# Performance work log

Hardware: AMD Instinct MI355X
Metric: run time of the kernel (lower is better)

Reference implementation:

```python
import jax, jax.numpy as jnp
import numpy as np

N_ANCHORS = 9
OUTPUT_STRIDE = 16
TOP_N = 2000
NMS_IOU_THRESH = 0.7
MIN_SIZE = 0.01
EPS = 1e-7  # K.epsilon()


def setup_inputs() -> dict:
    key = jax.random.key(0)
    k1, k2 = jax.random.split(key)
    b, h, w = 8, 64, 64  # 1024px image / stride 16
    scores = jax.random.uniform(k1, (b, h, w, N_ANCHORS), jnp.float32)
    offsets = jax.random.normal(k2, (b, h, w, 4 * N_ANCHORS), jnp.float32) * 0.2
    scales = np.array([128.0, 256.0, 512.0])
    ratios = np.array([0.5, 1.0, 2.0])
    aw = (scales[:, None] * np.sqrt(ratios)[None, :]).reshape(-1)
    ah = (scales[:, None] / np.sqrt(ratios)[None, :]).reshape(-1)
    anchors = jnp.asarray(np.stack([aw, ah], axis=-1), jnp.float32)  # [9,2]
    return {"scores": scores, "offsets": offsets, "anchors": anchors}


def _pairwise_iou(a, b):
    # a: [N,4], b: [M,4] (x1,y1,x2,y2) -> [N,M]
    a = a[:, None, :]
    b = b[None, :, :]
    mins = jnp.maximum(a[..., :2], b[..., :2])
    maxs = jnp.minimum(a[..., 2:], b[..., 2:])
    wh = jnp.maximum(maxs - mins, 0.0)
    inter = wh[..., 0] * wh[..., 1]
    area_a = (a[..., 2] - a[..., 0]) * (a[..., 3] - a[..., 1])
    area_b = (b[..., 2] - b[..., 0]) * (b[..., 3] - b[..., 1])
    return inter / (area_a + area_b - inter + EPS)


def _nms_pad(boxes):
    # boxes: [N,4] already sorted by descending score (output of top_k).
    # Greedy NMS (matches tf.image.non_max_suppression semantics), keep order,
    # zero-pad suppressed tail (matches tf.pad to top_n in the original).
    N = boxes.shape[0]
    iou = _pairwise_iou(boxes, boxes)  # [N,N]
    idx = jnp.arange(N)

    def body(i, keep):
        suppress = keep[i] & (iou[i] > NMS_IOU_THRESH) & (idx > i)
        return keep & ~suppress

    keep = jax.lax.fori_loop(0, N, body, jnp.ones((N,), bool))
    sort_keys = jnp.where(keep, idx, N)          # kept indices first, in score order
    order = jnp.argsort(sort_keys)
    valid = (jnp.sort(sort_keys) < N).astype(boxes.dtype)
    return boxes[order] * valid[:, None]


def reference(scores, offsets, anchors):
    b, h, w, K = scores.shape
    off = offsets.reshape(b, h, w, K, 4)
    # anchor decode
    gx, gy = jnp.meshgrid(jnp.arange(w), jnp.arange(h))          # [h,w] each
    center = (jnp.stack([gx, gy], -1).astype(jnp.float32) + 0.5) * OUTPUT_STRIDE  # [h,w,2]
    center = center[:, :, None, :]                               # [h,w,1,2]
    img_wh = jnp.array([w, h], jnp.float32) * OUTPUT_STRIDE
    anc = anchors.reshape(1, 1, 1, K, 2)
    pred_wh = jnp.exp(off[..., 2:]) * anc / img_wh               # [b,h,w,K,2]
    pred_xcyc = (anc * off[..., :2] + center) / img_wh
    box5 = jnp.concatenate([pred_xcyc - pred_wh / 2.0,
                            pred_xcyc + pred_wh / 2.0,
                            scores[..., None]], axis=-1)         # [b,h,w,K,5]
    # filter: clip to [0,1], zero out tiny boxes
    box5 = jnp.clip(box5, 0.0, 1.0)
    wh = box5[..., 2:4] - box5[..., 0:2]
    valid = ((wh[..., 0] > MIN_SIZE) & (wh[..., 1] > MIN_SIZE)).astype(box5.dtype)
    box5 = box5 * valid[..., None]
    box5 = box5.reshape(b, -1, 5)                                # [b, h*w*K, 5]
    # per-image top-k by score, then NMS, then zero-pad to TOP_N
    _, top_i = jax.lax.top_k(box5[..., 4], TOP_N)                # [b, TOP_N]
    top_boxes = jnp.take_along_axis(box5[..., :4], top_i[..., None], axis=1)
    proposals = jax.vmap(_nms_pad)(top_boxes)                    # [b, TOP_N, 4]
    return proposals
```

## Files before the change

kernel.cpp:

```cpp
#include <hip/hip_runtime.h>
#include <stdint.h>

#pragma clang fp contract(off)

#define BATCH 8
#define HH 64
#define WW 64
#define KA 9
#define NBOX (HH * WW * KA)
#define TOPN 2000
#define NPAD 2048
#define NW 32
#define IOU_T 0.7f
#define MINSZ 0.01f
#define EPSF 1e-7f
#define TSTRIDE 33
#define CANDCAP 3072

typedef unsigned int u32;
typedef unsigned long long u64;

__device__ __forceinline__ float clamp01(float x) { return fminf(fmaxf(x, 0.0f), 1.0f); }

__device__ __forceinline__ void bar_lds()
{
    asm volatile("s_waitcnt lgkmcnt(0)" ::: "memory");
    __builtin_amdgcn_s_barrier();
}

__device__ __forceinline__ void decode_one(
    const float* __restrict__ scores, const float4* __restrict__ offsets,
    const float* __restrict__ anchors, int gid, int t,
    float4* boxOut, u32* keyOut)
{
    int k = t % KA;
    int pos = t / KA;
    int wx = pos & (WW - 1);
    int hy = pos >> 6;
    float s = scores[gid];
    float4 off = offsets[gid];
    float aw = anchors[2 * k], ah = anchors[2 * k + 1];
    float cx = ((float)wx + 0.5f) * 16.0f;
    float cy = ((float)hy + 0.5f) * 16.0f;
    float pw = (expf(off.z) * aw) / 1024.0f;
    float ph = (expf(off.w) * ah) / 1024.0f;
    float xc = (aw * off.x + cx) / 1024.0f;
    float yc = (ah * off.y + cy) / 1024.0f;
    float x1 = clamp01(xc - pw * 0.5f);
    float y1 = clamp01(yc - ph * 0.5f);
    float x2 = clamp01(xc + pw * 0.5f);
    float y2 = clamp01(yc + ph * 0.5f);
    float sc = clamp01(s);
    float m = ((x2 - x1) > MINSZ && (y2 - y1) > MINSZ) ? 1.0f : 0.0f;
    *boxOut = make_float4(x1 * m, y1 * m, x2 * m, y2 * m);
    *keyOut = __float_as_uint(sc * m);
}

__global__ __launch_bounds__(256) void zero_kernel(uint4* __restrict__ p, int n)
{
    int g = blockIdx.x * 256 + threadIdx.x;
    if (g < n) p[g] = make_uint4(0, 0, 0, 0);
}

__global__ __launch_bounds__(256) void decode_kernel(
    const float* __restrict__ scores, const float4* __restrict__ offsets,
    const float* __restrict__ anchors, u32* __restrict__ keys,
    u32* __restrict__ ghist)
{
    __shared__ u32 lhist[4096];
    for (int i = threadIdx.x; i < 4096; i += 256) lhist[i] = 0;
    __syncthreads();

    int gid = blockIdx.x * 256 + threadIdx.x;
    int b = gid / NBOX;
    int t = gid - b * NBOX;
    float4 box; u32 key;
    decode_one(scores, offsets, anchors, gid, t, &box, &key);
    keys[gid] = key;
    atomicAdd(&lhist[key >> 20], 1u);
    __syncthreads();

    for (int i = threadIdx.x; i < 4096; i += 256) {
        u32 v = lhist[i];
        if (v) atomicAdd(&ghist[(b << 12) + i], v);
    }
}

__device__ __forceinline__ void rank_find_4096(
    const u32* __restrict__ histL, u32* __restrict__ partial,
    int r, u32* Bsh, int* Rsh, int tid)
{
    partial[tid] = histL[4 * tid] + histL[4 * tid + 1]
                 + histL[4 * tid + 2] + histL[4 * tid + 3];
    __syncthreads();
    if (tid < 64) {
        int lane = tid;
        u32 s = 0;
#pragma unroll
        for (int q = 0; q < 16; ++q) s += partial[lane * 16 + q];
        u32 suf = s;
#pragma unroll
        for (int d = 1; d < 64; d <<= 1) {
            u32 t = __shfl_down(suf, d);
            if (lane + d < 64) suf += t;
        }
        u32 nxt = __shfl_down(suf, 1);
        if (lane == 63) nxt = 0;
        bool cross = (suf >= (u32)r) && (nxt < (u32)r);
        u64 bal = __ballot(cross);
        int L = (int)(__ffsll((unsigned long long)bal) - 1);
        u32 above = __shfl(nxt, L);
        u32 hv = histL[64 * L + lane];
        u32 suf2 = hv;
#pragma unroll
        for (int d = 1; d < 64; d <<= 1) {
            u32 t = __shfl_down(suf2, d);
            if (lane + d < 64) suf2 += t;
        }
        u32 nxt2 = __shfl_down(suf2, 1);
        if (lane == 63) nxt2 = 0;
        u32 mine2 = suf2 + above;
        nxt2 += above;
        if (mine2 >= (u32)r && nxt2 < (u32)r) {
            *Bsh = (u32)(64 * L + lane);
            *Rsh = r - (int)nxt2;
        }
    }
    __syncthreads();
}

__global__ __launch_bounds__(1024) void select_kernel(
    const u32* __restrict__ keys, const u32* __restrict__ ghist,
    const float* __restrict__ scores, const float4* __restrict__ offsets,
    const float* __restrict__ anchors, float4* __restrict__ topBoxes)
{
    int b = blockIdx.x;
    int tid = threadIdx.x;
    int lane = tid & 63;
    const u32* kb = keys + (size_t)b * NBOX;

    __shared__ u32 hist[4096];
    __shared__ u32 partial[1024];
    __shared__ u64 sel[NPAD];
    __shared__ u64 cand[CANDCAP];
    __shared__ u32 Bsh;
    __shared__ int Rsh;
    __shared__ int ctr, cctr;

    if (tid == 0) { ctr = 0; cctr = 0; }
    for (int i = tid; i < 4096; i += 1024) hist[i] = ghist[(b << 12) + i];
    for (int i = tid; i < NPAD; i += 1024) sel[i] = 0ull;
    __syncthreads();
    rank_find_4096(hist, partial, TOPN, &Bsh, &Rsh, tid);
    u32 P1 = Bsh;
    int r1 = Rsh;
    __syncthreads();

    const uint4* kb4 = (const uint4*)kb;
#pragma unroll 1
    for (int it = 0; it < NBOX / 4096; ++it) {
        int i4 = it * 1024 + tid;
        uint4 kv = kb4[i4];
        u32 karr[4] = { kv.x, kv.y, kv.z, kv.w };
        u64 bd[4], bc[4];
        int totd = 0, totc = 0;
#pragma unroll
        for (int q = 0; q < 4; ++q) {
            u32 top = karr[q] >> 20;
            bd[q] = __ballot(top > P1);
            bc[q] = __ballot(top == P1);
            totd += (int)__popcll(bd[q]);
            totc += (int)__popcll(bc[q]);
        }
        int based = 0, basec = 0;
        if (lane == 0) {
            if (totd) based = atomicAdd(&ctr, totd);
            if (totc) basec = atomicAdd(&cctr, totc);
        }
        based = __shfl(based, 0);
        basec = __shfl(basec, 0);
        u64 lmask = (1ull << lane) - 1ull;
        int offd = 0, offc = 0;
#pragma unroll
        for (int q = 0; q < 4; ++q) {
            u32 key = karr[q];
            int i = i4 * 4 + q;
            u64 K = ((u64)key << 16) | (u64)(0xFFFFu - (u32)i);
            u32 top = key >> 20;
            if (top > P1) {
                int slot = based + offd + (int)__popcll(bd[q] & lmask);
                if (slot < NPAD) sel[slot] = K;
            } else if (top == P1) {
                int cslot = basec + offc + (int)__popcll(bc[q] & lmask);
                if (cslot < CANDCAP) cand[cslot] = K;
            }
            offd += (int)__popcll(bd[q]);
            offc += (int)__popcll(bc[q]);
        }
    }
    __syncthreads();
    int cc = cctr < CANDCAP ? cctr : CANDCAP;

    u64 prefix = (u64)P1;
    int r = r1;
    for (int p = 0; p < 3; ++p) {
        int shift = 24 - 12 * p;
        for (int i = tid; i < 4096; i += 1024) hist[i] = 0;
        __syncthreads();
        for (int c = tid; c < cc; c += 1024) {
            u64 K = cand[c];
            if ((K >> (shift + 12)) == prefix)
                atomicAdd(&hist[(u32)((K >> shift) & 0xFFFull)], 1u);
        }
        __syncthreads();
        rank_find_4096(hist, partial, r, &Bsh, &Rsh, tid);
        prefix = (prefix << 12) | (u64)Bsh;
        r = Rsh;
        __syncthreads();
    }
    u64 T48 = prefix;

    for (int c = tid; c < cc; c += 1024) {
        u64 K = cand[c];
        bool take = (K >= T48);
        u64 bal = __ballot(take);
        int base = 0;
        if (lane == 0 && bal) base = atomicAdd(&ctr, (int)__popcll(bal));
        base = __shfl(base, 0);
        if (take) {
            int slot = base + (int)__popcll(bal & ((1ull << lane) - 1ull));
            if (slot < NPAD) sel[slot] = K;
        }
    }
    __syncthreads();

    u64 e0 = sel[tid];
    u64 e1 = sel[tid + 1024];
    const int i0 = tid, i1 = tid + 1024;

    for (int k = 2; k <= NPAD; k <<= 1) {
        for (int j = k >> 1; j >= 64; j >>= 1) {
            if (j == 1024) {
                u64 mx = e0 > e1 ? e0 : e1;
                u64 mn = e0 > e1 ? e1 : e0;
                e0 = mx; e1 = mn;
            } else {
                sel[i0] = e0; sel[i1] = e1;
                __syncthreads();
                u64 p0 = sel[i0 ^ j];
                u64 p1 = sel[i1 ^ j];
                bool kp0 = ((i0 & k) == 0) ^ ((i0 & j) != 0);
                bool kp1 = ((i1 & k) == 0) ^ ((i1 & j) != 0);
                e0 = kp0 ? (e0 > p0 ? e0 : p0) : (e0 < p0 ? e0 : p0);
                e1 = kp1 ? (e1 > p1 ? e1 : p1) : (e1 < p1 ? e1 : p1);
                __syncthreads();
            }
        }
        int jstart = (k >> 1) < 32 ? (k >> 1) : 32;
        for (int j = jstart; j >= 1; j >>= 1) {
            u64 p0 = __shfl_xor(e0, j);
            u64 p1 = __shfl_xor(e1, j);
            bool kp0 = ((i0 & k) == 0) ^ ((i0 & j) != 0);
            bool kp1 = ((i1 & k) == 0) ^ ((i1 & j) != 0);
            e0 = kp0 ? (e0 > p0 ? e0 : p0) : (e0 < p0 ? e0 : p0);
            e1 = kp1 ? (e1 > p1 ? e1 : p1) : (e1 < p1 ? e1 : p1);
        }
    }

    {
        float4 v; u32 kd;
        int idx = 0xFFFF - (int)(e0 & 0xFFFFull);
        decode_one(scores, offsets, anchors, b * NBOX + idx, idx, &v, &kd);
        topBoxes[b * NPAD + i0] = v;
    }
    {
        float4 v = make_float4(0, 0, 0, 0);
        if (i1 < TOPN) {
            u32 kd;
            int idx = 0xFFFF - (int)(e1 & 0xFFFFull);
            decode_one(scores, offsets, anchors, b * NBOX + idx, idx, &v, &kd);
        }
        topBoxes[b * NPAD + i1] = v;
    }
}

__global__ __launch_bounds__(256) void iou_kernel(
    const float4* __restrict__ topBoxes, u64* __restrict__ sup)
{
    int gid = blockIdx.x * 256 + threadIdx.x;
    int wid = gid >> 6;
    int lane = gid & 63;
    int b = wid / TOPN;
    int r = wid - b * TOPN;

    float4 A = topBoxes[(size_t)b * NPAD + r];
    float areaA = (A.z - A.x) * (A.w - A.y);
    size_t supBase = ((size_t)b * NPAD + r) * NW;

    for (int w = r >> 6; w < NW; ++w) {
        int j = w * 64 + lane;
        float4 Bx = topBoxes[(size_t)b * NPAD + j];
        float ix1 = fmaxf(A.x, Bx.x);
        float iy1 = fmaxf(A.y, Bx.y);
        float ix2 = fminf(A.z, Bx.z);
        float iy2 = fminf(A.w, Bx.w);
        float iw = fmaxf(ix2 - ix1, 0.0f);
        float ih = fmaxf(iy2 - iy1, 0.0f);
        float inter = iw * ih;
        float areaB = (Bx.z - Bx.x) * (Bx.w - Bx.y);
        float iou = inter / (areaA + areaB - inter + EPSF);
        bool s = (iou > IOU_T) && (j > r) && (j < TOPN);
        u64 m = __ballot(s);
        if (lane == 0) sup[supBase + w] = m;
    }
}

__global__ __launch_bounds__(256) void resolve_kernel(
    const u64* __restrict__ sup, const float4* __restrict__ topBoxes,
    float4* __restrict__ out)
{
    int b = blockIdx.x;
    int tid = threadIdx.x;
    __shared__ u64 tile[2][64 * TSTRIDE];
    __shared__ u64 keep[NW];
    __shared__ u64 nzmap[NW];
    __shared__ int wbase[NW];
    if (tid < NW) keep[tid] = (tid < 31) ? ~0ull : 0xFFFFull;
    const u64* supB = sup + (size_t)b * NPAD * NW;
    unsigned* keep32 = (unsigned*)keep;

    int row = tid >> 2;
    int wcol = (tid & 3) * 8;

    {
        const uint4* src = (const uint4*)(supB + tid * 8);
        uint4 p0 = src[0], p1 = src[1], p2 = src[2], p3 = src[3];
        u64* d = &tile[0][row * TSTRIDE + wcol];
        d[0] = ((u64)p0.y << 32) | p0.x;  d[1] = ((u64)p0.w << 32) | p0.z;
        d[2] = ((u64)p1.y << 32) | p1.x;  d[3] = ((u64)p1.w << 32) | p1.z;
        d[4] = ((u64)p2.y << 32) | p2.x;  d[5] = ((u64)p2.w << 32) | p2.z;
        d[6] = ((u64)p3.y << 32) | p3.x;  d[7] = ((u64)p3.w << 32) | p3.z;
    }
    bar_lds();

    for (int w = 0; w < NW; ++w) {
        int buf = w & 1;
        uint4 n0, n1, n2, n3;
        if (w + 1 < NW) {
            const uint4* src = (const uint4*)(supB + (size_t)(w + 1) * 2048 + tid * 8);
            n0 = src[0]; n1 = src[1]; n2 = src[2]; n3 = src[3];
        }

        if (tid < 64) {
            u64 m = tile[buf][tid * TSTRIDE + w];
            u64 later = 0;
            for (int w2 = w + 1; w2 < NW; ++w2) later |= tile[buf][tid * TSTRIDE + w2];
            u64 nzAny = __ballot((m | later) != 0ull);
            u64 nzDiag = __ballot(m != 0ull);
            u32 mlo = (u32)m, mhi = (u32)(m >> 32);
            u64 kw64 = keep[w];
            u32 kwlo = (u32)__builtin_amdgcn_readfirstlane((int)(u32)kw64);
            u32 kwhi = (u32)__builtin_amdgcn_readfirstlane((int)(u32)(kw64 >> 32));
            u64 kw = ((u64)kwhi << 32) | kwlo;
            u64 rem = kw & nzDiag;
            while (rem) {
                int t2 = (int)(__ffsll((unsigned long long)rem) - 1);
                u32 alo = (u32)__builtin_amdgcn_readlane((int)mlo, t2);
                u32 ahi = (u32)__builtin_amdgcn_readlane((int)mhi, t2);
                u64 mt = ((u64)ahi << 32) | alo;
                kw &= ~mt;
                rem &= ~(mt | (1ull << t2));
            }
            if (tid == 0) { keep[w] = kw; nzmap[w] = nzAny; }
        }
        bar_lds();

        u64 gate = keep[w] & nzmap[w];
        int w2 = tid & 31;
        int grp = tid >> 5;
        if (w2 > w && gate) {
            u64 acc = 0;
#pragma unroll
            for (int q = 0; q < 8; ++q) {
                int rl = grp * 8 + q;
                if ((gate >> rl) & 1ull)
                    acc |= tile[buf][rl * TSTRIDE + w2];
            }
            if (acc) {
                u32 lo = (u32)acc, hi = (u32)(acc >> 32);
                if (lo) atomicAnd(&keep32[2 * w2], ~lo);
                if (hi) atomicAnd(&keep32[2 * w2 + 1], ~hi);
            }
        }

        if (w + 1 < NW) {
            u64* d = &tile[buf ^ 1][row * TSTRIDE + wcol];
            d[0] = ((u64)n0.y << 32) | n0.x;  d[1] = ((u64)n0.w << 32) | n0.z;
            d[2] = ((u64)n1.y << 32) | n1.x;  d[3] = ((u64)n1.w << 32) | n1.z;
            d[4] = ((u64)n2.y << 32) | n2.x;  d[5] = ((u64)n2.w << 32) | n2.z;
            d[6] = ((u64)n3.y << 32) | n3.x;  d[7] = ((u64)n3.w << 32) | n3.z;
        }
        bar_lds();
    }

    if (tid == 0) {
        int s = 0;
        for (int w2 = 0; w2 < NW; ++w2) { wbase[w2] = s; s += __popcll(keep[w2]); }
    }
    __syncthreads();
    for (int i = tid; i < TOPN; i += 256)
        out[(size_t)b * TOPN + i] = make_float4(0, 0, 0, 0);
    __syncthreads();
    for (int i = tid; i < TOPN; i += 256) {
        int wi = i >> 6, bz = i & 63;
        u64 kw = keep[wi];
        if ((kw >> bz) & 1ull) {
            int pos = wbase[wi] + __popcll(kw & ((1ull << bz) - 1ull));
            out[(size_t)b * TOPN + pos] = topBoxes[(size_t)b * NPAD + i];
        }
    }
}

extern "C" void kernel_launch(void* const* d_in, const int* in_sizes, int n_in,
                              void* d_out, int out_size, void* d_ws, size_t ws_size,
                              hipStream_t stream)
{
    const float*  scores  = (const float*)d_in[0];
    const float4* offsets = (const float4*)d_in[1];
    const float*  anchors = (const float*)d_in[2];
    float4* out = (float4*)d_out;

    char* ws = (char*)d_ws;
    u64*    sup      = (u64*)(ws);
    u32*    keys     = (u32*)(ws + 4194304);
    float4* topBoxes = (float4*)(ws + 5373952);
    u32*    ghist    = (u32*)(ws + 5636096);

    zero_kernel<<<(131072 / 16 + 255) / 256, 256, 0, stream>>>((uint4*)ghist, 131072 / 16);
    decode_kernel<<<(BATCH * NBOX) / 256, 256, 0, stream>>>(scores, offsets, anchors, keys, ghist);
    select_kernel<<<BATCH, 1024, 0, stream>>>(keys, ghist, scores, offsets, anchors, topBoxes);
    iou_kernel<<<(BATCH * TOPN * 64) / 256, 256, 0, stream>>>(topBoxes, sup);
    resolve_kernel<<<BATCH, 256, 0, stream>>>(sup, topBoxes, out);
}
```

Measured before the change: 106.4 us.

## Split select kernel into scan, grid-wide compaction, and final refine kernels

The single per-image select kernel (8 blocks) is replaced by three kernels. A small scan kernel finds the top radix bucket, a compact kernel over 288 blocks filters keys into global selected and candidate buffers using global atomics, and a final kernel refines the threshold and sorts. The aim is to spread the memory-bound key scan across many CUs instead of 8. In exchange it adds two launches, global atomics, and a global round trip for the candidates, and the zeroed workspace region grows.

```diff
diff --git a/kernel.cpp b/kernel.cpp
--- a/kernel.cpp
+++ b/kernel.cpp
@@ -15,7 +15,7 @@
 #define MINSZ 0.01f
 #define EPSF 1e-7f
 #define TSTRIDE 33
-#define CANDCAP 3072
+#define CANDCAP 4096
 
 typedef unsigned int u32;
 typedef unsigned long long u64;
@@ -129,77 +129,98 @@
     __syncthreads();
 }
 
-__global__ __launch_bounds__(1024) void select_kernel(
-    const u32* __restrict__ keys, const u32* __restrict__ ghist,
+__global__ __launch_bounds__(1024) void scan_kernel(
+    const u32* __restrict__ ghist, u32* __restrict__ P, int* __restrict__ R)
+{
+    int b = blockIdx.x, tid = threadIdx.x;
+    __shared__ u32 hist[4096];
+    __shared__ u32 partial[1024];
+    __shared__ u32 Bsh;
+    __shared__ int Rsh;
+    for (int i = tid; i < 4096; i += 1024) hist[i] = ghist[(b << 12) + i];
+    __syncthreads();
+    rank_find_4096(hist, partial, TOPN, &Bsh, &Rsh, tid);
+    if (tid == 0) { P[b] = Bsh; R[b] = Rsh; }
+}
+
+__global__ __launch_bounds__(256) void compact_kernel(
+    const u32* __restrict__ keys, const u32* __restrict__ P,
+    int* __restrict__ ctr, int* __restrict__ cctr,
+    u64* __restrict__ selKeys, u64* __restrict__ candG)
+{
+    int bid = blockIdx.x;
+    int b = bid / 36;
+    int blk = bid - b * 36;
+    int tid = threadIdx.x;
+    int lane = tid & 63;
+    u32 P1 = P[b];
+
+    int i4 = blk * 256 + tid;
+    const uint4* kb4 = (const uint4*)(keys + (size_t)b * NBOX);
+    uint4 kv = kb4[i4];
+    u32 karr[4] = { kv.x, kv.y, kv.z, kv.w };
+    u64 bd[4], bc[4];
+    int totd = 0, totc = 0;
+#pragma unroll
+    for (int q = 0; q < 4; ++q) {
+        u32 top = karr[q] >> 20;
+        bd[q] = __ballot(top > P1);
+        bc[q] = __ballot(top == P1);
+        totd += (int)__popcll(bd[q]);
+        totc += (int)__popcll(bc[q]);
+    }
+    int based = 0, basec = 0;
+    if (lane == 0) {
+        if (totd) based = atomicAdd(&ctr[b], totd);
+        if (totc) basec = atomicAdd(&cctr[b], totc);
+    }
+    based = __shfl(based, 0);
+    basec = __shfl(basec, 0);
+    u64 lmask = (1ull << lane) - 1ull;
+    int offd = 0, offc = 0;
+#pragma unroll
+    for (int q = 0; q < 4; ++q) {
+        u32 key = karr[q];
+        int i = i4 * 4 + q;
+        u64 K = ((u64)key << 16) | (u64)(0xFFFFu - (u32)i);
+        u32 top = key >> 20;
+        if (top > P1) {
+            int slot = based + offd + (int)__popcll(bd[q] & lmask);
+            if (slot < NPAD) selKeys[(size_t)b * NPAD + slot] = K;
+        } else if (top == P1) {
+            int cslot = basec + offc + (int)__popcll(bc[q] & lmask);
+            if (cslot < CANDCAP) candG[(size_t)b * CANDCAP + cslot] = K;
+        }
+        offd += (int)__popcll(bd[q]);
+        offc += (int)__popcll(bc[q]);
+    }
+}
+
+__global__ __launch_bounds__(1024) void final_kernel(
+    const u64* __restrict__ selKeysG, const u64* __restrict__ candG,
+    const u32* __restrict__ P, const int* __restrict__ R,
+    const int* __restrict__ ctr, const int* __restrict__ cctr,
     const float* __restrict__ scores, const float4* __restrict__ offsets,
     const float* __restrict__ anchors, float4* __restrict__ topBoxes)
 {
     int b = blockIdx.x;
     int tid = threadIdx.x;
     int lane = tid & 63;
-    const u32* kb = keys + (size_t)b * NBOX;
 
     __shared__ u32 hist[4096];
     __shared__ u32 partial[1024];
     __shared__ u64 sel[NPAD];
-    __shared__ u64 cand[CANDCAP];
     __shared__ u32 Bsh;
     __shared__ int Rsh;
-    __shared__ int ctr, cctr;
-
-    if (tid == 0) { ctr = 0; cctr = 0; }
-    for (int i = tid; i < 4096; i += 1024) hist[i] = ghist[(b << 12) + i];
-    for (int i = tid; i < NPAD; i += 1024) sel[i] = 0ull;
-    __syncthreads();
-    rank_find_4096(hist, partial, TOPN, &Bsh, &Rsh, tid);
-    u32 P1 = Bsh;
-    int r1 = Rsh;
-    __syncthreads();
-
-    const uint4* kb4 = (const uint4*)kb;
-#pragma unroll 1
-    for (int it = 0; it < NBOX / 4096; ++it) {
-        int i4 = it * 1024 + tid;
-        uint4 kv = kb4[i4];
-        u32 karr[4] = { kv.x, kv.y, kv.z, kv.w };
-        u64 bd[4], bc[4];
-        int totd = 0, totc = 0;
-#pragma unroll
-        for (int q = 0; q < 4; ++q) {
-            u32 top = karr[q] >> 20;
-            bd[q] = __ballot(top > P1);
-            bc[q] = __ballot(top == P1);
-            totd += (int)__popcll(bd[q]);
-            totc += (int)__popcll(bc[q]);
-        }
-        int based = 0, basec = 0;
-        if (lane == 0) {
-            if (totd) based = atomicAdd(&ctr, totd);
-            if (totc) basec = atomicAdd(&cctr, totc);
-        }
-        based = __shfl(based, 0);
-        basec = __shfl(basec, 0);
-        u64 lmask = (1ull << lane) - 1ull;
-        int offd = 0, offc = 0;
-#pragma unroll
-        for (int q = 0; q < 4; ++q) {
-            u32 key = karr[q];
-            int i = i4 * 4 + q;
-            u64 K = ((u64)key << 16) | (u64)(0xFFFFu - (u32)i);
-            u32 top = key >> 20;
-            if (top > P1) {
-                int slot = based + offd + (int)__popcll(bd[q] & lmask);
-                if (slot < NPAD) sel[slot] = K;
-            } else if (top == P1) {
-                int cslot = basec + offc + (int)__popcll(bc[q] & lmask);
-                if (cslot < CANDCAP) cand[cslot] = K;
-            }
-            offd += (int)__popcll(bd[q]);
-            offc += (int)__popcll(bc[q]);
-        }
-    }
-    __syncthreads();
-    int cc = cctr < CANDCAP ? cctr : CANDCAP;
+    __shared__ int ctr2;
+
+    sel[tid]        = selKeysG[(size_t)b * NPAD + tid];
+    sel[tid + 1024] = selKeysG[(size_t)b * NPAD + tid + 1024];
+    if (tid == 0) ctr2 = ctr[b];
+    int cc = cctr[b]; cc = cc < CANDCAP ? cc : CANDCAP;
+    u32 P1 = P[b];
+    int r1 = R[b];
+    const u64* cb = candG + (size_t)b * CANDCAP;
 
     u64 prefix = (u64)P1;
     int r = r1;
@@ -208,7 +229,7 @@
         for (int i = tid; i < 4096; i += 1024) hist[i] = 0;
         __syncthreads();
         for (int c = tid; c < cc; c += 1024) {
-            u64 K = cand[c];
+            u64 K = cb[c];
             if ((K >> (shift + 12)) == prefix)
                 atomicAdd(&hist[(u32)((K >> shift) & 0xFFFull)], 1u);
         }
@@ -221,11 +242,11 @@
     u64 T48 = prefix;
 
     for (int c = tid; c < cc; c += 1024) {
-        u64 K = cand[c];
+        u64 K = cb[c];
         bool take = (K >= T48);
         u64 bal = __ballot(take);
         int base = 0;
-        if (lane == 0 && bal) base = atomicAdd(&ctr, (int)__popcll(bal));
+        if (lane == 0 && bal) base = atomicAdd(&ctr2, (int)__popcll(bal));
         base = __shfl(base, 0);
         if (take) {
             int slot = base + (int)__popcll(bal & ((1ull << lane) - 1ull));
@@ -434,11 +455,21 @@
     u64*    sup      = (u64*)(ws);
     u32*    keys     = (u32*)(ws + 4194304);
     float4* topBoxes = (float4*)(ws + 5373952);
-    u32*    ghist    = (u32*)(ws + 5636096);
-
-    zero_kernel<<<(131072 / 16 + 255) / 256, 256, 0, stream>>>((uint4*)ghist, 131072 / 16);
+    u64*    candG    = (u64*)(ws + 5636096);
+    u32*    ghist    = (u32*)(ws + 5898240);
+    u64*    selKeys  = (u64*)(ws + 6029312);
+    u32*    P        = (u32*)(ws + 6160384);
+    int*    R        = (int*)(ws + 6160384 + 32);
+    int*    ctr      = (int*)(ws + 6160384 + 64);
+    int*    cctr     = (int*)(ws + 6160384 + 96);
+
+    const int ZERO_N = 262400 / 16;
+    zero_kernel<<<(ZERO_N + 255) / 256, 256, 0, stream>>>((uint4*)(ws + 5898240), ZERO_N);
     decode_kernel<<<(BATCH * NBOX) / 256, 256, 0, stream>>>(scores, offsets, anchors, keys, ghist);
-    select_kernel<<<BATCH, 1024, 0, stream>>>(keys, ghist, scores, offsets, anchors, topBoxes);
+    scan_kernel<<<BATCH, 1024, 0, stream>>>(ghist, P, R);
+    compact_kernel<<<BATCH * 36, 256, 0, stream>>>(keys, P, ctr, cctr, selKeys, candG);
+    final_kernel<<<BATCH, 1024, 0, stream>>>(selKeys, candG, P, R, ctr, cctr,
+                                             scores, offsets, anchors, topBoxes);
     iou_kernel<<<(BATCH * TOPN * 64) / 256, 256, 0, stream>>>(topBoxes, sup);
     resolve_kernel<<<BATCH, 256, 0, stream>>>(sup, topBoxes, out);
 }
```

After: 117.6 us. +10.5%, slower.

## Resolve NMS by walking only rows that suppress something, using wave-register keep mask

Applied to the files above, without the earlier changes.

The IoU kernel now records a per-row flag marking whether a box suppresses anything. It writes that row's 32 suppression words only when the flag is set, with one lane storing each word instead of a store per word-column. The resolve kernel compacts the flagged rows into a list in LDS. A single wave then walks that list serially, holding the keep mask as 64 32-bit lanes, using readlane to test whether each row is still kept and prefetching suppression words 8 ahead. This replaces the double-buffered tile pass over the full matrix with its per-word barriers, at the cost of a serial dependent loop whose length scales with the number of overlapping rows.

```diff
diff --git a/kernel.cpp b/kernel.cpp
--- a/kernel.cpp
+++ b/kernel.cpp
@@ -14,19 +14,12 @@
 #define IOU_T 0.7f
 #define MINSZ 0.01f
 #define EPSF 1e-7f
-#define TSTRIDE 33
 #define CANDCAP 3072
 
 typedef unsigned int u32;
 typedef unsigned long long u64;
 
 __device__ __forceinline__ float clamp01(float x) { return fminf(fmaxf(x, 0.0f), 1.0f); }
-
-__device__ __forceinline__ void bar_lds()
-{
-    asm volatile("s_waitcnt lgkmcnt(0)" ::: "memory");
-    __builtin_amdgcn_s_barrier();
-}
 
 __device__ __forceinline__ void decode_one(
     const float* __restrict__ scores, const float4* __restrict__ offsets,
@@ -285,7 +278,8 @@
 }
 
 __global__ __launch_bounds__(256) void iou_kernel(
-    const float4* __restrict__ topBoxes, u64* __restrict__ sup)
+    const float4* __restrict__ topBoxes, u64* __restrict__ sup,
+    unsigned char* __restrict__ rowNZ)
 {
     int gid = blockIdx.x * 256 + threadIdx.x;
     int wid = gid >> 6;
@@ -297,6 +291,7 @@
     float areaA = (A.z - A.x) * (A.w - A.y);
     size_t supBase = ((size_t)b * NPAD + r) * NW;
 
+    u64 msave = 0, anyM = 0;
     for (int w = r >> 6; w < NW; ++w) {
         int j = w * 64 + lane;
         float4 Bx = topBoxes[(size_t)b * NPAD + j];
@@ -311,101 +306,85 @@
         float iou = inter / (areaA + areaB - inter + EPSF);
         bool s = (iou > IOU_T) && (j > r) && (j < TOPN);
         u64 m = __ballot(s);
-        if (lane == 0) sup[supBase + w] = m;
-    }
+        anyM |= m;
+        if (lane == w) msave = m;
+    }
+    if (lane == 0) rowNZ[(size_t)b * NPAD + r] = anyM ? 1 : 0;
+    if (anyM && lane < NW) sup[supBase + lane] = msave;
 }
 
 __global__ __launch_bounds__(256) void resolve_kernel(
-    const u64* __restrict__ sup, const float4* __restrict__ topBoxes,
-    float4* __restrict__ out)
+    const u64* __restrict__ sup, const unsigned char* __restrict__ rowNZ,
+    const float4* __restrict__ topBoxes, float4* __restrict__ out)
 {
     int b = blockIdx.x;
     int tid = threadIdx.x;
-    __shared__ u64 tile[2][64 * TSTRIDE];
-    __shared__ u64 keep[NW];
-    __shared__ u64 nzmap[NW];
+    int lane = tid & 63;
+    int wv = tid >> 6;
+
+    __shared__ unsigned short supList[TOPN];
+    __shared__ int wt[4];
+    __shared__ int chunkBase;
+    __shared__ u32 keep32[64];
     __shared__ int wbase[NW];
-    if (tid < NW) keep[tid] = (tid < 31) ? ~0ull : 0xFFFFull;
-    const u64* supB = sup + (size_t)b * NPAD * NW;
-    unsigned* keep32 = (unsigned*)keep;
-
-    int row = tid >> 2;
-    int wcol = (tid & 3) * 8;
-
-    {
-        const uint4* src = (const uint4*)(supB + tid * 8);
-        uint4 p0 = src[0], p1 = src[1], p2 = src[2], p3 = src[3];
-        u64* d = &tile[0][row * TSTRIDE + wcol];
-        d[0] = ((u64)p0.y << 32) | p0.x;  d[1] = ((u64)p0.w << 32) | p0.z;
-        d[2] = ((u64)p1.y << 32) | p1.x;  d[3] = ((u64)p1.w << 32) | p1.z;
-        d[4] = ((u64)p2.y << 32) | p2.x;  d[5] = ((u64)p2.w << 32) | p2.z;
-        d[6] = ((u64)p3.y << 32) | p3.x;  d[7] = ((u64)p3.w << 32) | p3.z;
-    }
-    bar_lds();
-
-    for (int w = 0; w < NW; ++w) {
-        int buf = w & 1;
-        uint4 n0, n1, n2, n3;
-        if (w + 1 < NW) {
-            const uint4* src = (const uint4*)(supB + (size_t)(w + 1) * 2048 + tid * 8);
-            n0 = src[0]; n1 = src[1]; n2 = src[2]; n3 = src[3];
-        }
-
-        if (tid < 64) {
-            u64 m = tile[buf][tid * TSTRIDE + w];
-            u64 later = 0;
-            for (int w2 = w + 1; w2 < NW; ++w2) later |= tile[buf][tid * TSTRIDE + w2];
-            u64 nzAny = __ballot((m | later) != 0ull);
-            u64 nzDiag = __ballot(m != 0ull);
-            u32 mlo = (u32)m, mhi = (u32)(m >> 32);
-            u64 kw64 = keep[w];
-            u32 kwlo = (u32)__builtin_amdgcn_readfirstlane((int)(u32)kw64);
-            u32 kwhi = (u32)__builtin_amdgcn_readfirstlane((int)(u32)(kw64 >> 32));
-            u64 kw = ((u64)kwhi << 32) | kwlo;
-            u64 rem = kw & nzDiag;
-            while (rem) {
-                int t2 = (int)(__ffsll((unsigned long long)rem) - 1);
-                u32 alo = (u32)__builtin_amdgcn_readlane((int)mlo, t2);
-                u32 ahi = (u32)__builtin_amdgcn_readlane((int)mhi, t2);
-                u64 mt = ((u64)ahi << 32) | alo;
-                kw &= ~mt;
-                rem &= ~(mt | (1ull << t2));
-            }
-            if (tid == 0) { keep[w] = kw; nzmap[w] = nzAny; }
-        }
-        bar_lds();
-
-        u64 gate = keep[w] & nzmap[w];
-        int w2 = tid & 31;
-        int grp = tid >> 5;
-        if (w2 > w && gate) {
-            u64 acc = 0;
-#pragma unroll
-            for (int q = 0; q < 8; ++q) {
-                int rl = grp * 8 + q;
-                if ((gate >> rl) & 1ull)
-                    acc |= tile[buf][rl * TSTRIDE + w2];
-            }
-            if (acc) {
-                u32 lo = (u32)acc, hi = (u32)(acc >> 32);
-                if (lo) atomicAnd(&keep32[2 * w2], ~lo);
-                if (hi) atomicAnd(&keep32[2 * w2 + 1], ~hi);
-            }
-        }
-
-        if (w + 1 < NW) {
-            u64* d = &tile[buf ^ 1][row * TSTRIDE + wcol];
-            d[0] = ((u64)n0.y << 32) | n0.x;  d[1] = ((u64)n0.w << 32) | n0.z;
-            d[2] = ((u64)n1.y << 32) | n1.x;  d[3] = ((u64)n1.w << 32) | n1.z;
-            d[4] = ((u64)n2.y << 32) | n2.x;  d[5] = ((u64)n2.w << 32) | n2.z;
-            d[6] = ((u64)n3.y << 32) | n3.x;  d[7] = ((u64)n3.w << 32) | n3.z;
-        }
-        bar_lds();
-    }
-
+
+    if (tid == 0) chunkBase = 0;
+    __syncthreads();
+
+    const unsigned char* nzB = rowNZ + (size_t)b * NPAD;
+    for (int c = 0; c < 8; ++c) {
+        int r = c * 256 + tid;
+        bool nz = (r < TOPN) && (nzB[r] != 0);
+        u64 bal = __ballot(nz);
+        if (lane == 0) wt[wv] = (int)__popcll(bal);
+        __syncthreads();
+        int before = 0;
+        for (int q = 0; q < wv; ++q) before += wt[q];
+        if (nz) {
+            int slot = chunkBase + before + (int)__popcll(bal & ((1ull << lane) - 1ull));
+            supList[slot] = (unsigned short)r;
+        }
+        __syncthreads();
+        if (tid == 0) chunkBase += wt[0] + wt[1] + wt[2] + wt[3];
+        __syncthreads();
+    }
+    int S = chunkBase;
+
+    if (tid < 64) {
+        u32 kseg = (lane < 62) ? 0xFFFFFFFFu : (lane == 62 ? 0xFFFFu : 0u);
+        const u32* rows = (const u32*)(sup + (size_t)b * NPAD * NW);
+
+#define LOADG(dst, pos) dst = ((pos) < S) ? rows[(size_t)supList[(pos)] * 64 + lane] : 0u;
+#define STEP(cc, pos)                                                          \
+        if ((pos) < S) {                                                       \
+            int ii = supList[(pos)];                                           \
+            u32 bit = (u32)__builtin_amdgcn_readlane((int)kseg, ii >> 5)       \
+                      & (1u << (ii & 31));                                     \
+            if (bit) kseg &= ~(cc);                                            \
+        }
+
+        u32 c0, c1, c2, c3, c4, c5, c6, c7;
+        LOADG(c0, 0) LOADG(c1, 1) LOADG(c2, 2) LOADG(c3, 3)
+        LOADG(c4, 4) LOADG(c5, 5) LOADG(c6, 6) LOADG(c7, 7)
+        for (int g = 0; g < S; g += 8) {
+            u32 n0, n1, n2, n3, n4, n5, n6, n7;
+            LOADG(n0, g + 8)  LOADG(n1, g + 9)  LOADG(n2, g + 10) LOADG(n3, g + 11)
+            LOADG(n4, g + 12) LOADG(n5, g + 13) LOADG(n6, g + 14) LOADG(n7, g + 15)
+            STEP(c0, g)     STEP(c1, g + 1) STEP(c2, g + 2) STEP(c3, g + 3)
+            STEP(c4, g + 4) STEP(c5, g + 5) STEP(c6, g + 6) STEP(c7, g + 7)
+            c0 = n0; c1 = n1; c2 = n2; c3 = n3;
+            c4 = n4; c5 = n5; c6 = n6; c7 = n7;
+        }
+#undef LOADG
+#undef STEP
+        keep32[lane] = kseg;
+    }
+    __syncthreads();
+
+    const u64* keep64 = (const u64*)keep32;
     if (tid == 0) {
         int s = 0;
-        for (int w2 = 0; w2 < NW; ++w2) { wbase[w2] = s; s += __popcll(keep[w2]); }
+        for (int w2 = 0; w2 < NW; ++w2) { wbase[w2] = s; s += __popcll(keep64[w2]); }
     }
     __syncthreads();
     for (int i = tid; i < TOPN; i += 256)
@@ -413,7 +392,7 @@
     __syncthreads();
     for (int i = tid; i < TOPN; i += 256) {
         int wi = i >> 6, bz = i & 63;
-        u64 kw = keep[wi];
+        u64 kw = keep64[wi];
         if ((kw >> bz) & 1ull) {
             int pos = wbase[wi] + __popcll(kw & ((1ull << bz) - 1ull));
             out[(size_t)b * TOPN + pos] = topBoxes[(size_t)b * NPAD + i];
@@ -431,14 +410,15 @@
     float4* out = (float4*)d_out;
 
     char* ws = (char*)d_ws;
-    u64*    sup      = (u64*)(ws);
-    u32*    keys     = (u32*)(ws + 4194304);
-    float4* topBoxes = (float4*)(ws + 5373952);
-    u32*    ghist    = (u32*)(ws + 5636096);
+    u64*           sup      = (u64*)(ws);
+    u32*           keys     = (u32*)(ws + 4194304);
+    float4*        topBoxes = (float4*)(ws + 5373952);
+    u32*           ghist    = (u32*)(ws + 5636096);
+    unsigned char* rowNZ    = (unsigned char*)(ws + 5767168);
 
     zero_kernel<<<(131072 / 16 + 255) / 256, 256, 0, stream>>>((uint4*)ghist, 131072 / 16);
     decode_kernel<<<(BATCH * NBOX) / 256, 256, 0, stream>>>(scores, offsets, anchors, keys, ghist);
     select_kernel<<<BATCH, 1024, 0, stream>>>(keys, ghist, scores, offsets, anchors, topBoxes);
-    iou_kernel<<<(BATCH * TOPN * 64) / 256, 256, 0, stream>>>(topBoxes, sup);
-    resolve_kernel<<<BATCH, 256, 0, stream>>>(sup, topBoxes, out);
-}
+    iou_kernel<<<(BATCH * TOPN * 64) / 256, 256, 0, stream>>>(topBoxes, sup, rowNZ);
+    resolve_kernel<<<BATCH, 256, 0, stream>>>(sup, rowNZ, topBoxes, out);
+}
```

After: 177.8 us. 67.1% more time.

## Record per-row nonzero flags in IoU kernel and skip empty suppression rows

Applied to the files above, without the earlier changes.

The IoU kernel now keeps each 64-bit suppression mask in the lane matching its word index. It writes the whole row in one coalesced store, and only when the row has any suppression bit set. It also emits a per-row nonzero byte. The resolve kernel packs these bytes into nzmap up front, so it can skip global loads of empty rows and drop the per-step scan over later words that used to rebuild nzmap. This cuts serial work and memory traffic in the single-block-per-image resolve stage. The cost is an extra byte array and the reliance on unwritten padding rows being masked by keep.

```diff
diff --git a/kernel.cpp b/kernel.cpp
--- a/kernel.cpp
+++ b/kernel.cpp
@@ -285,7 +285,8 @@
 }
 
 __global__ __launch_bounds__(256) void iou_kernel(
-    const float4* __restrict__ topBoxes, u64* __restrict__ sup)
+    const float4* __restrict__ topBoxes, u64* __restrict__ sup,
+    unsigned char* __restrict__ rowNZ)
 {
     int gid = blockIdx.x * 256 + threadIdx.x;
     int wid = gid >> 6;
@@ -297,6 +298,7 @@
     float areaA = (A.z - A.x) * (A.w - A.y);
     size_t supBase = ((size_t)b * NPAD + r) * NW;
 
+    u64 msave = 0, anyM = 0;
     for (int w = r >> 6; w < NW; ++w) {
         int j = w * 64 + lane;
         float4 Bx = topBoxes[(size_t)b * NPAD + j];
@@ -311,30 +313,50 @@
         float iou = inter / (areaA + areaB - inter + EPSF);
         bool s = (iou > IOU_T) && (j > r) && (j < TOPN);
         u64 m = __ballot(s);
-        if (lane == 0) sup[supBase + w] = m;
-    }
+        anyM |= m;
+        if (lane == w) msave = m;
+    }
+    if (lane == 0) rowNZ[(size_t)b * NPAD + r] = anyM ? 1 : 0;
+    if (anyM && lane < NW) sup[supBase + lane] = msave;
 }
 
 __global__ __launch_bounds__(256) void resolve_kernel(
-    const u64* __restrict__ sup, const float4* __restrict__ topBoxes,
-    float4* __restrict__ out)
+    const u64* __restrict__ sup, const unsigned char* __restrict__ rowNZ,
+    const float4* __restrict__ topBoxes, float4* __restrict__ out)
 {
     int b = blockIdx.x;
     int tid = threadIdx.x;
     __shared__ u64 tile[2][64 * TSTRIDE];
     __shared__ u64 keep[NW];
     __shared__ u64 nzmap[NW];
+    __shared__ unsigned char nzbytes[256];
     __shared__ int wbase[NW];
     if (tid < NW) keep[tid] = (tid < 31) ? ~0ull : 0xFFFFull;
     const u64* supB = sup + (size_t)b * NPAD * NW;
+    const unsigned char* nzB = rowNZ + (size_t)b * NPAD;
     unsigned* keep32 = (unsigned*)keep;
+
+    {
+        u64 v = ((const u64*)nzB)[tid];
+        u32 bits = 0;
+#pragma unroll
+        for (int q = 0; q < 8; ++q)
+            bits |= (((v >> (8 * q)) & 0xFFull) ? 1u : 0u) << q;
+        nzbytes[tid] = (unsigned char)bits;
+    }
+    __syncthreads();
+    if (tid < NW) nzmap[tid] = ((const u64*)nzbytes)[tid];
+    __syncthreads();
 
     int row = tid >> 2;
     int wcol = (tid & 3) * 8;
 
     {
-        const uint4* src = (const uint4*)(supB + tid * 8);
-        uint4 p0 = src[0], p1 = src[1], p2 = src[2], p3 = src[3];
+        uint4 p0 = make_uint4(0, 0, 0, 0), p1 = p0, p2 = p0, p3 = p0;
+        if ((nzmap[0] >> row) & 1ull) {
+            const uint4* src = (const uint4*)(supB + tid * 8);
+            p0 = src[0]; p1 = src[1]; p2 = src[2]; p3 = src[3];
+        }
         u64* d = &tile[0][row * TSTRIDE + wcol];
         d[0] = ((u64)p0.y << 32) | p0.x;  d[1] = ((u64)p0.w << 32) | p0.z;
         d[2] = ((u64)p1.y << 32) | p1.x;  d[3] = ((u64)p1.w << 32) | p1.z;
@@ -345,17 +367,14 @@
 
     for (int w = 0; w < NW; ++w) {
         int buf = w & 1;
-        uint4 n0, n1, n2, n3;
-        if (w + 1 < NW) {
+        uint4 n0 = make_uint4(0, 0, 0, 0), n1 = n0, n2 = n0, n3 = n0;
+        if (w + 1 < NW && ((nzmap[w + 1] >> row) & 1ull)) {
             const uint4* src = (const uint4*)(supB + (size_t)(w + 1) * 2048 + tid * 8);
             n0 = src[0]; n1 = src[1]; n2 = src[2]; n3 = src[3];
         }
 
         if (tid < 64) {
             u64 m = tile[buf][tid * TSTRIDE + w];
-            u64 later = 0;
-            for (int w2 = w + 1; w2 < NW; ++w2) later |= tile[buf][tid * TSTRIDE + w2];
-            u64 nzAny = __ballot((m | later) != 0ull);
             u64 nzDiag = __ballot(m != 0ull);
             u32 mlo = (u32)m, mhi = (u32)(m >> 32);
             u64 kw64 = keep[w];
@@ -371,7 +390,7 @@
                 kw &= ~mt;
                 rem &= ~(mt | (1ull << t2));
             }
-            if (tid == 0) { keep[w] = kw; nzmap[w] = nzAny; }
+            if (tid == 0) keep[w] = kw;
         }
         bar_lds();
 
@@ -431,14 +450,15 @@
     float4* out = (float4*)d_out;
 
     char* ws = (char*)d_ws;
-    u64*    sup      = (u64*)(ws);
-    u32*    keys     = (u32*)(ws + 4194304);
-    float4* topBoxes = (float4*)(ws + 5373952);
-    u32*    ghist    = (u32*)(ws + 5636096);
+    u64*           sup      = (u64*)(ws);
+    u32*           keys     = (u32*)(ws + 4194304);
+    float4*        topBoxes = (float4*)(ws + 5373952);
+    u32*           ghist    = (u32*)(ws + 5636096);
+    unsigned char* rowNZ    = (unsigned char*)(ws + 5767168);
 
     zero_kernel<<<(131072 / 16 + 255) / 256, 256, 0, stream>>>((uint4*)ghist, 131072 / 16);
     decode_kernel<<<(BATCH * NBOX) / 256, 256, 0, stream>>>(scores, offsets, anchors, keys, ghist);
     select_kernel<<<BATCH, 1024, 0, stream>>>(keys, ghist, scores, offsets, anchors, topBoxes);
-    iou_kernel<<<(BATCH * TOPN * 64) / 256, 256, 0, stream>>>(topBoxes, sup);
-    resolve_kernel<<<BATCH, 256, 0, stream>>>(sup, topBoxes, out);
-}
+    iou_kernel<<<(BATCH * TOPN * 64) / 256, 256, 0, stream>>>(topBoxes, sup, rowNZ);
+    resolve_kernel<<<BATCH, 256, 0, stream>>>(sup, rowNZ, topBoxes, out);
+}
```

New measurement: 114.6 us. 1.08x slower.
